# Kernel tuning notes

Hardware: AMD Instinct MI355X
Metric: run time of the kernel (lower is better)

The kernel has to match this reference:

```python
import jax, jax.numpy as jnp
import numpy as np

NUM_HEADS = 16
HEAD_DIM = 80  # head_dim_ori; NPU pads 80->128 with zeros (math-neutral)


def _rotate_half(x):
    x1, x2 = jnp.split(x, 2, axis=-1)
    return jnp.concatenate([-x2, x1], axis=-1)


def setup_inputs() -> dict:
    key = jax.random.key(0)
    ks = jax.random.split(key, 7)
    S, E = 4096, 1280
    inv = jnp.asarray(1.0 / np.sqrt(E), jnp.float32)
    # rotary tables: proper cos/sin from angles for realism
    pos = jnp.arange(S, dtype=jnp.float32)[:, None]
    freqs = 1.0 / (10000.0 ** (jnp.arange(0, HEAD_DIM // 2, dtype=jnp.float32) / (HEAD_DIM // 2)))
    ang = pos * freqs[None, :]                      # [S, 40]
    ang = jnp.concatenate([ang, ang], axis=-1)      # [S, 80] rotate-half layout
    return {
        'hidden_states': jax.random.normal(ks[0], (S, E), jnp.float32),
        'cos': jnp.cos(ang),
        'sin': jnp.sin(ang),
        'w_qkv': jax.random.normal(ks[1], (3 * E, E), jnp.float32) * inv,
        'b_qkv': jax.random.normal(ks[2], (3 * E,), jnp.float32) * 0.02,
        'w_proj': jax.random.normal(ks[3], (E, E), jnp.float32) * inv,
        'b_proj': jax.random.normal(ks[4], (E,), jnp.float32) * 0.02,
    }


def reference(hidden_states, cos, sin, w_qkv, b_qkv, w_proj, b_proj):
    S, E = hidden_states.shape
    H, D = NUM_HEADS, HEAD_DIM
    # fused QKV linear (transposeB=True, hasBias=True) then split into 3
    qkv = hidden_states @ w_qkv.T + b_qkv          # [S, 3E]
    q, k, v = jnp.split(qkv, 3, axis=-1)
    q = q.reshape(S, H, D)
    k = k.reshape(S, H, D)
    v = v.reshape(S, H, D)
    # rotate-half RoPE (rotaryCoeff=2) on q and k
    c = cos[:, None, :]
    s = sin[:, None, :]
    q = q * c + _rotate_half(q) * s
    k = k * c + _rotate_half(k) * s
    # full bidirectional self-attention (PA_ENCODER), qkScale = 1/sqrt(head_dim_ori)
    scale = jnp.asarray(1.0 / np.sqrt(D), q.dtype)
    scores = jnp.einsum('shd,thd->hst', q, k) * scale   # [H, S, S]
    attn = jax.nn.softmax(scores, axis=-1)
    out = jnp.einsum('hst,thd->shd', attn, v).reshape(S, E)
    # output projection + residual add (atten_res_add)
    dense = out @ w_proj.T + b_proj
    return hidden_states + dense
```

## Files before the change

### kernel.cpp

```cpp
#include <hip/hip_runtime.h>
#include <hip/hip_bf16.h>


#define S_LEN 4096
#define E_DIM 1280
#define NH 16
#define HD 80
#define HDP 96

typedef __bf16 bf16x8 __attribute__((ext_vector_type(8)));
typedef float f32x4 __attribute__((ext_vector_type(4)));

__device__ __forceinline__ short f2bf(float x) {
    __hip_bfloat16 h = __float2bfloat16(x);
    return __builtin_bit_cast(short, h);
}
__device__ __forceinline__ bf16x8 ldb(const short* p) {
    return *reinterpret_cast<const bf16x8*>(p);
}
__device__ __forceinline__ unsigned cvt_pk_bf16(float a, float b) {
    unsigned r;
    asm("v_cvt_pk_bf16_f32 %0, %1, %2" : "=v"(r) : "v"(a), "v"(b));
    return r;
}
__device__ __forceinline__ void gload16(const void* g, void* l) {
    __builtin_amdgcn_global_load_lds(
        (const __attribute__((address_space(1))) unsigned int*)g,
        (__attribute__((address_space(3))) unsigned int*)l, 16, 0, 0);
}

__global__ __launch_bounds__(256) void cast3_k(const float* __restrict__ a, short* __restrict__ oa, int na4,
                                               const float* __restrict__ b, short* __restrict__ ob, int nb4,
                                               const float* __restrict__ c, short* __restrict__ oc, int nc4) {
    int j = blockIdx.x * 256 + threadIdx.x;
    const float* src;
    short* dst;
    bool remap = false;
    if (j < na4) {
        src = a; dst = oa;
    } else {
        j -= na4;
        if (j < nb4) {
            src = b; dst = ob; remap = true;
        } else {
            j -= nb4;
            if (j >= nc4) return;
            src = c; dst = oc;
        }
    }
    float4 v = *reinterpret_cast<const float4*>(&src[j * 4]);
    int dj = j;
    if (remap) {
        int row = j / 320, c4 = j - row * 320;
        if (row < 2560) {
            int part = row / 1280;
            int loc = row - part * 1280;
            int hh = loc / 80, d = loc - hh * 80;
            int dp = (d < 40) ? 2 * d : 2 * (d - 40) + 1;
            dj = (part * 1280 + hh * 80 + dp) * 320 + c4;
        }
    }
    ushort4 o;
    o.x = (unsigned short)f2bf(v.x);
    o.y = (unsigned short)f2bf(v.y);
    o.z = (unsigned short)f2bf(v.z);
    o.w = (unsigned short)f2bf(v.w);
    *reinterpret_cast<ushort4*>(&dst[dj * 4]) = o;
}

__global__ __launch_bounds__(512, 2) void gemm1_256_k(
    const short* __restrict__ A, const short* __restrict__ B, const float* __restrict__ bias,
    const float* __restrict__ cosp, const float* __restrict__ sinp,
    short* __restrict__ Qg, short* __restrict__ Kg, short* __restrict__ Vg) {
    const int K = E_DIM;
    __shared__ short As[2][2][8192];
    __shared__ short Bs[2][2][8192];
    int t = threadIdx.x;
    int lane = t & 63, w = t >> 6;
    int wr = w >> 2, wc = w & 3;
    int lr = lane & 15, lg = lane >> 4;
    int bid = blockIdx.x;
    int swz = (bid & 7) * 30 + (bid >> 3);
    int bm = swz / 15, bn = swz % 15;
    int mb = bm * 256, nb = bn * 256;

    int lgs = (t & 3) ^ ((t >> 3) & 3);
    const short* aS = A + (size_t)(mb + (t >> 2)) * K + lgs * 8;
    const short* bS = B + (size_t)(nb + (t >> 2)) * K + lgs * 8;
    const int rowStep = 128 * K;

    int aoff[2][4], boff[4];
#pragma unroll
    for (int mq = 0; mq < 2; mq++)
#pragma unroll
        for (int ii = 0; ii < 4; ii++) {
            int r = wr * 128 + mq * 64 + ii * 16 + lr;
            aoff[mq][ii] = r * 32 + ((lg ^ ((r >> 1) & 3)) * 8);
        }
#pragma unroll
    for (int n = 0; n < 4; n++) {
        int r = wc * 64 + n * 16 + lr;
        boff[n] = r * 32 + ((lg ^ ((r >> 1) & 3)) * 8);
    }

    f32x4 acc[8][4];
#pragma unroll
    for (int i = 0; i < 8; i++)
#pragma unroll
        for (int n = 0; n < 4; n++) acc[i][n] = (f32x4){0.f, 0.f, 0.f, 0.f};

#define STG_A(d, kh, kb2)                                              \
    {                                                                  \
        gload16(aS + (kb2) + (kh)*32, &As[d][kh][w * 512]);            \
        gload16(aS + rowStep + (kb2) + (kh)*32, &As[d][kh][4096 + w * 512]); \
    }
#define STG_B(d, kh, kb2)                                              \
    {                                                                  \
        gload16(bS + (kb2) + (kh)*32, &Bs[d][kh][w * 512]);            \
        gload16(bS + rowStep + (kb2) + (kh)*32, &Bs[d][kh][4096 + w * 512]); \
    }

    STG_A(0, 0, 0);
    STG_B(0, 0, 0);
    STG_A(0, 1, 0);
    STG_B(0, 1, 0);
    asm volatile("s_waitcnt vmcnt(4)" ::: "memory");
    __builtin_amdgcn_s_barrier();
    asm volatile("" ::: "memory");

    for (int kb = 0; kb < K; kb += 64) {
        int d = (kb >> 6) & 1;
        int kb2 = kb + 64;
        bool more = kb2 < K;
        bf16x8 af[4], bfr[4];

#pragma unroll
        for (int n = 0; n < 4; n++) bfr[n] = ldb(&Bs[d][0][boff[n]]);
#pragma unroll
        for (int ii = 0; ii < 4; ii++) af[ii] = ldb(&As[d][0][aoff[0][ii]]);
        if (more) STG_A(d ^ 1, 0, kb2);
        __builtin_amdgcn_s_barrier();
        asm volatile("s_waitcnt lgkmcnt(0)" ::: "memory");
        __builtin_amdgcn_sched_barrier(0);
        __builtin_amdgcn_s_setprio(1);
#pragma unroll
        for (int ii = 0; ii < 4; ii++)
#pragma unroll
            for (int n = 0; n < 4; n++)
                acc[ii][n] = __builtin_amdgcn_mfma_f32_16x16x32_bf16(af[ii], bfr[n], acc[ii][n], 0, 0, 0);
        __builtin_amdgcn_s_setprio(0);
        __builtin_amdgcn_s_barrier();
        asm volatile("" ::: "memory");

#pragma unroll
        for (int ii = 0; ii < 4; ii++) af[ii] = ldb(&As[d][0][aoff[1][ii]]);
        if (more) {
            STG_B(d ^ 1, 0, kb2);
            asm volatile("s_waitcnt vmcnt(4)" ::: "memory");
        } else {
            asm volatile("s_waitcnt vmcnt(0)" ::: "memory");
        }
        __builtin_amdgcn_s_barrier();
        asm volatile("s_waitcnt lgkmcnt(0)" ::: "memory");
        __builtin_amdgcn_sched_barrier(0);
        __builtin_amdgcn_s_setprio(1);
#pragma unroll
        for (int ii = 0; ii < 4; ii++)
#pragma unroll
            for (int n = 0; n < 4; n++)
                acc[4 + ii][n] = __builtin_amdgcn_mfma_f32_16x16x32_bf16(af[ii], bfr[n], acc[4 + ii][n], 0, 0, 0);
        __builtin_amdgcn_s_setprio(0);
        __builtin_amdgcn_s_barrier();
        asm volatile("" ::: "memory");

#pragma unroll
        for (int n = 0; n < 4; n++) bfr[n] = ldb(&Bs[d][1][boff[n]]);
#pragma unroll
        for (int ii = 0; ii < 4; ii++) af[ii] = ldb(&As[d][1][aoff[0][ii]]);
        if (more) STG_A(d ^ 1, 1, kb2);
        __builtin_amdgcn_s_barrier();
        asm volatile("s_waitcnt lgkmcnt(0)" ::: "memory");
        __builtin_amdgcn_sched_barrier(0);
        __builtin_amdgcn_s_setprio(1);
#pragma unroll
        for (int ii = 0; ii < 4; ii++)
#pragma unroll
            for (int n = 0; n < 4; n++)
                acc[ii][n] = __builtin_amdgcn_mfma_f32_16x16x32_bf16(af[ii], bfr[n], acc[ii][n], 0, 0, 0);
        __builtin_amdgcn_s_setprio(0);
        __builtin_amdgcn_s_barrier();
        asm volatile("" ::: "memory");

#pragma unroll
        for (int ii = 0; ii < 4; ii++) af[ii] = ldb(&As[d][1][aoff[1][ii]]);
        if (more) {
            STG_B(d ^ 1, 1, kb2);
            asm volatile("s_waitcnt vmcnt(4)" ::: "memory");
        }
        __builtin_amdgcn_s_barrier();
        asm volatile("s_waitcnt lgkmcnt(0)" ::: "memory");
        __builtin_amdgcn_sched_barrier(0);
        __builtin_amdgcn_s_setprio(1);
#pragma unroll
        for (int ii = 0; ii < 4; ii++)
#pragma unroll
            for (int n = 0; n < 4; n++)
                acc[4 + ii][n] = __builtin_amdgcn_mfma_f32_16x16x32_bf16(af[ii], bfr[n], acc[4 + ii][n], 0, 0, 0);
        __builtin_amdgcn_s_setprio(0);
        __builtin_amdgcn_s_barrier();
        asm volatile("" ::: "memory");
    }
#undef STG_A
#undef STG_B

    int part = nb / E_DIM;
    if (part < 2) {
        short* dst = part ? Kg : Qg;
        const float scl = part ? 1.0f : 0.16129849190f;
#pragma unroll
        for (int j = 0; j < 4; j++) {
            int cn = wc * 64 + j * 16 + lr;
            int pcol = nb - part * E_DIM + cn;
            int hh = pcol / 80;
            int dl = pcol - hh * 80;
            int i2 = dl >> 1;
            int parity = dl & 1;
            float bv = bias[part * E_DIM + hh * 80 + (parity ? i2 + 40 : i2)];
            size_t hbase = (size_t)hh * S_LEN * HDP;
#pragma unroll
            for (int i = 0; i < 8; i++) {
#pragma unroll
                for (int r = 0; r < 4; r++) {
                    int s = mb + wr * 128 + (i >> 2) * 64 + (i & 3) * 16 + lg * 4 + r;
                    float v = acc[i][j][r] + bv;
                    float pv = __shfl_xor(v, 1);
                    float cc = cosp[s * HD + i2];
                    float ss = sinp[s * HD + i2];
                    float ov = fmaf(v, cc, parity ? pv * ss : -pv * ss) * scl;
                    size_t rowb = hbase + (size_t)s * HDP;
                    dst[rowb + dl] = f2bf(ov);
                    if (dl >= 64) dst[rowb + dl + 16] = 0;
                }
            }
        }
    } else {
#pragma unroll
        for (int j = 0; j < 4; j++) {
            int cn = wc * 64 + j * 16 + lr;
            float bv = bias[nb + cn];
            int col = nb - 2 * E_DIM + cn;
#pragma unroll
            for (int i = 0; i < 8; i++) {
#pragma unroll
                for (int r = 0; r < 4; r++) {
                    int s = mb + wr * 128 + (i >> 2) * 64 + (i & 3) * 16 + lg * 4 + r;
                    Vg[(size_t)s * E_DIM + col] = f2bf(acc[i][j][r] + bv);
                }
            }
        }
    }
}

__global__ __launch_bounds__(256) void gemm_bt_k(
    const short* __restrict__ A, const short* __restrict__ B, const float* __restrict__ bias,
    const float* __restrict__ resid, float* __restrict__ Out) {
    const int K = E_DIM;
    __shared__ short As[2][128 * 64];
    __shared__ short Bs[2][128 * 64];
    int t = threadIdx.x;
    int lane = t & 63, w = t >> 6;
    int wr = w >> 1, wc = w & 1;
    int lr = lane & 15, lg = lane >> 4;
    int mb = blockIdx.y * 128, nb = blockIdx.x * 128;

    const short* asrc[4];
    const short* bsrc[4];
#pragma unroll
    for (int c = 0; c < 4; c++) {
        int p = c * 256 + t;
        int m = p >> 3;
        int kg = (p & 7) ^ (m & 7);
        asrc[c] = A + (size_t)(mb + m) * K + kg * 8;
        bsrc[c] = B + (size_t)(nb + m) * K + kg * 8;
    }
    int xa = lr & 7;
    int cx0 = ((0 * 4 + lg) ^ xa) * 8;
    int cx1 = ((1 * 4 + lg) ^ xa) * 8;
    int rowA[4], rowB[4];
#pragma unroll
    for (int i = 0; i < 4; i++) {
        rowA[i] = (wr * 64 + i * 16 + lr) * 64;
        rowB[i] = (wc * 64 + i * 16 + lr) * 64;
    }

    f32x4 acc[4][4];
#pragma unroll
    for (int i = 0; i < 4; i++)
#pragma unroll
        for (int j = 0; j < 4; j++) acc[i][j] = (f32x4){0.f, 0.f, 0.f, 0.f};

#define G_STAGE(buf, kb)                                             \
    {                                                                \
        _Pragma("unroll") for (int c = 0; c < 4; c++) {              \
            int ldso = c * 2048 + w * 512;                           \
            gload16(asrc[c] + (kb), &As[buf][ldso]);                 \
            gload16(bsrc[c] + (kb), &Bs[buf][ldso]);                 \
        }                                                            \
    }

    G_STAGE(0, 0);
    asm volatile("s_waitcnt vmcnt(0)" ::: "memory");
    __syncthreads();

    int buf = 0;
    for (int kb = 0; kb < K; kb += 64) {
        if (kb + 64 < K) G_STAGE(buf ^ 1, kb + 64);
        __builtin_amdgcn_s_setprio(1);
#pragma unroll
        for (int kk = 0; kk < 2; kk++) {
            int cx = kk ? cx1 : cx0;
            bf16x8 af[4], bfr[4];
#pragma unroll
            for (int i = 0; i < 4; i++) {
                af[i] = ldb(&As[buf][rowA[i] + cx]);
                bfr[i] = ldb(&Bs[buf][rowB[i] + cx]);
            }
#pragma unroll
            for (int i = 0; i < 4; i++)
#pragma unroll
                for (int j = 0; j < 4; j++)
                    acc[i][j] = __builtin_amdgcn_mfma_f32_16x16x32_bf16(af[i], bfr[j], acc[i][j], 0, 0, 0);
        }
        __builtin_amdgcn_s_setprio(0);
        __syncthreads();
        buf ^= 1;
    }
#undef G_STAGE

#pragma unroll
    for (int j = 0; j < 4; j++) {
        int n = nb + wc * 64 + j * 16 + lr;
        float bv = bias[n];
#pragma unroll
        for (int i = 0; i < 4; i++) {
#pragma unroll
            for (int r = 0; r < 4; r++) {
                int s = mb + wr * 64 + i * 16 + lg * 4 + r;
                Out[s * E_DIM + n] = acc[i][j][r] + bv + resid[s * E_DIM + n];
            }
        }
    }
}

__global__ __launch_bounds__(256) void transpose_v_k(const short* __restrict__ Vg,
                                                     short* __restrict__ Vt) {
    __shared__ short tile[32][33];
    int h = blockIdx.z, sb = blockIdx.x * 32, db = blockIdx.y * 32;
    int t = threadIdx.x;
    for (int e = t; e < 1024; e += 256) {
        int si = e >> 5, dj = e & 31;
        int d = db + dj;
        tile[si][dj] = (d < HD) ? Vg[(size_t)(sb + si) * E_DIM + h * HD + d] : (short)0;
    }
    __syncthreads();
    for (int e = t; e < 1024; e += 256) {
        int di = e >> 5, sj = e & 31;
        int d = db + di;
        int pj = ((sj >> 2) & 3) * 8 + ((sj >> 4) & 1) * 4 + (sj & 3);
        if (d < HD) Vt[(h * HD + d) * S_LEN + sb + pj] = tile[sj][di];
    }
}

__global__ __launch_bounds__(512, 4) void attn_k(const short* __restrict__ Qg,
                                                 const short* __restrict__ Kg,
                                                 const short* __restrict__ Vt,
                                                 short* __restrict__ Ob) {
    __shared__ __align__(16) short smem[24832];
    short* ksb = smem;
    short* vsb = smem + 13312;

    int t = threadIdx.x;
    int lane = t & 63, w = t >> 6;
    int lr = lane & 15, lg = lane >> 4;
    int pairi = w >> 1, half = w & 1;
    int L = blockIdx.x;
    int h = ((L & 7) << 1) | (L >> 8);
    int qb = ((L >> 3) & 31) << 7;

    const short* kgp = Kg + (size_t)h * S_LEN * HDP;
    const short* vgp = Vt + (size_t)h * HD * S_LEN;

    bf16x8 qf[2][3];
#pragma unroll
    for (int qq = 0; qq < 2; qq++) {
        const short* qp = Qg + ((size_t)h * S_LEN + qb + pairi * 32 + qq * 16 + lr) * HDP;
#pragma unroll
        for (int kk = 0; kk < 3; kk++) qf[qq][kk] = ldb(qp + kk * 32 + lg * 8);
    }
    f32x4 o[2][5];
#pragma unroll
    for (int qq = 0; qq < 2; qq++)
#pragma unroll
        for (int nd = 0; nd < 5; nd++) o[qq][nd] = (f32x4){0.f, 0.f, 0.f, 0.f};
    f32x4 l4[2] = {(f32x4){0.f, 0.f, 0.f, 0.f}, (f32x4){0.f, 0.f, 0.f, 0.f}};

    int gk0 = t, rk0 = gk0 / 13, ok0 = gk0 % 13;
    if (ok0 == 12) ok0 = 0;
    const short* ksrc0 = kgp + rk0 * HDP + ok0 * 8;
    int gk1 = t + 512, rk1 = gk1 / 13, ok1 = gk1 % 13;
    if (ok1 == 12) ok1 = 0;
    const short* ksrc1 = kgp + rk1 * HDP + ok1 * 8;
    int gv0 = t, rv0 = gv0 / 9, ov0 = gv0 % 9;
    if (ov0 == 8) ov0 = 0;
    const short* vsrc0 = vgp + (size_t)rv0 * S_LEN + ov0 * 8;
    bool v1v = (t + 512) < 720;
    int gv1 = t + 512, rv1 = gv1 / 9, ov1 = gv1 % 9;
    if (ov1 == 8) ov1 = 0;
    const short* vsrc1 = vgp + (size_t)rv1 * S_LEN + ov1 * 8;

#define A_STAGE(buf, kb)                                                          \
    {                                                                             \
        gload16(ksrc0 + (size_t)(kb) * HDP, ksb + (buf)*6656 + w * 512);          \
        if (w < 5) gload16(ksrc1 + (size_t)(kb) * HDP, ksb + (buf)*6656 + 4096 + w * 512); \
        gload16(vsrc0 + (kb), vsb + (buf)*5760 + w * 512);                        \
        if (v1v) gload16(vsrc1 + (kb), vsb + (buf)*5760 + 4096 + w * 512);        \
    }

    A_STAGE(0, 0);
    asm volatile("s_waitcnt vmcnt(0)" ::: "memory");
    __syncthreads();

    int buf = 0;
    for (int kb = 0; kb < S_LEN; kb += 64) {
        if (kb + 64 < S_LEN) A_STAGE(buf ^ 1, kb + 64);
        const short* ks = ksb + buf * 6656;
        const short* vs = vsb + buf * 5760;

        f32x4 sc[2][2];
#pragma unroll
        for (int qq = 0; qq < 2; qq++)
#pragma unroll
            for (int n = 0; n < 2; n++) sc[qq][n] = (f32x4){0.f, 0.f, 0.f, 0.f};
        __builtin_amdgcn_s_setprio(1);
#pragma unroll
        for (int n = 0; n < 2; n++) {
#pragma unroll
            for (int kk = 0; kk < 3; kk++) {
                bf16x8 kf = ldb(&ks[(half * 32 + n * 16 + lr) * 104 + kk * 32 + lg * 8]);
                sc[0][n] = __builtin_amdgcn_mfma_f32_16x16x32_bf16(kf, qf[0][kk], sc[0][n], 0, 0, 0);
                sc[1][n] = __builtin_amdgcn_mfma_f32_16x16x32_bf16(kf, qf[1][kk], sc[1][n], 0, 0, 0);
            }
        }
        __builtin_amdgcn_s_setprio(0);

        bf16x8 pa[2];
#pragma unroll
        for (int qq = 0; qq < 2; qq++) {
#pragma unroll
            for (int n = 0; n < 2; n++) {
#pragma unroll
                for (int r = 0; r < 4; r++) sc[qq][n][r] = __builtin_amdgcn_exp2f(sc[qq][n][r]);
                l4[qq] += sc[qq][n];
            }
            uint4 pw;
            pw.x = cvt_pk_bf16(sc[qq][0][0], sc[qq][0][1]);
            pw.y = cvt_pk_bf16(sc[qq][0][2], sc[qq][0][3]);
            pw.z = cvt_pk_bf16(sc[qq][1][0], sc[qq][1][1]);
            pw.w = cvt_pk_bf16(sc[qq][1][2], sc[qq][1][3]);
            pa[qq] = __builtin_bit_cast(bf16x8, pw);
        }

        __builtin_amdgcn_s_setprio(1);
#pragma unroll
        for (int nd = 0; nd < 5; nd++) {
            bf16x8 vf = ldb(&vs[(nd * 16 + lr) * 72 + half * 32 + lg * 8]);
            o[0][nd] = __builtin_amdgcn_mfma_f32_16x16x32_bf16(pa[0], vf, o[0][nd], 0, 0, 0);
            o[1][nd] = __builtin_amdgcn_mfma_f32_16x16x32_bf16(pa[1], vf, o[1][nd], 0, 0, 0);
        }
        __builtin_amdgcn_s_setprio(0);

        __syncthreads();
        buf ^= 1;
    }
#undef A_STAGE

    float lh[2];
#pragma unroll
    for (int qq = 0; qq < 2; qq++) {
        float l = l4[qq][0] + l4[qq][1] + l4[qq][2] + l4[qq][3];
        l += __shfl_xor(l, 16);
        l += __shfl_xor(l, 32);
        lh[qq] = l;
    }
    float* Osc = reinterpret_cast<float*>(smem);
    float* lsc = reinterpret_cast<float*>(smem) + 10240;
    if (half) {
#pragma unroll
        for (int qq = 0; qq < 2; qq++) {
#pragma unroll
            for (int nd = 0; nd < 5; nd++)
#pragma unroll
                for (int r = 0; r < 4; r++)
                    Osc[(pairi * 32 + qq * 16 + lg * 4 + r) * 80 + nd * 16 + lr] = o[qq][nd][r];
            if (lg == 0) lsc[pairi * 32 + qq * 16 + lr] = lh[qq];
        }
    }
    __syncthreads();
    if (!half) {
        float rl[2][4];
#pragma unroll
        for (int qq = 0; qq < 2; qq++) {
            float lt = lh[qq] + lsc[pairi * 32 + qq * 16 + lr];
#pragma unroll
            for (int r = 0; r < 4; r++) {
                float lf = __shfl(lt, lg * 4 + r);
                rl[qq][r] = __builtin_amdgcn_rcpf(lf);
            }
        }
#pragma unroll
        for (int qq = 0; qq < 2; qq++)
#pragma unroll
            for (int nd = 0; nd < 5; nd++)
#pragma unroll
                for (int r = 0; r < 4; r++) {
                    int s = qb + pairi * 32 + qq * 16 + lg * 4 + r;
                    float val = o[qq][nd][r] + Osc[(pairi * 32 + qq * 16 + lg * 4 + r) * 80 + nd * 16 + lr];
                    Ob[s * E_DIM + h * HD + nd * 16 + lr] = f2bf(val * rl[qq][r]);
                }
    }
}

extern "C" void kernel_launch(void* const* d_in, const int* in_sizes, int n_in,
                              void* d_out, int out_size, void* d_ws, size_t ws_size,
                              hipStream_t stream) {
    const float* hidden = (const float*)d_in[0];
    const float* cosp = (const float*)d_in[1];
    const float* sinp = (const float*)d_in[2];
    const float* wqkv = (const float*)d_in[3];
    const float* bqkv = (const float*)d_in[4];
    const float* wproj = (const float*)d_in[5];
    const float* bproj = (const float*)d_in[6];
    float* out = (float*)d_out;

    char* p = (char*)d_ws;
    short* Xb = (short*)p;      p += (size_t)S_LEN * E_DIM * 2;
    short* Wqkvb = (short*)p;   p += (size_t)3 * E_DIM * E_DIM * 2;
    short* Wprojb = (short*)p;  p += (size_t)E_DIM * E_DIM * 2;
    short* Vg = (short*)p;      p += (size_t)S_LEN * E_DIM * 2;
    short* Qg = (short*)p;      p += (size_t)NH * S_LEN * HDP * 2;
    short* Kg = (short*)p;      p += (size_t)NH * S_LEN * HDP * 2;
    short* Vt = (short*)p;      p += (size_t)NH * HD * S_LEN * 2;
    short* Ob = Xb;

    const int na4 = S_LEN * E_DIM / 4;
    const int nb4 = 3 * E_DIM * E_DIM / 4;
    const int nc4 = E_DIM * E_DIM / 4;
    cast3_k<<<(na4 + nb4 + nc4 + 255) / 256, 256, 0, stream>>>(
        hidden, Xb, na4, wqkv, Wqkvb, nb4, wproj, Wprojb, nc4);

    gemm1_256_k<<<dim3(240), 512, 0, stream>>>(Xb, Wqkvb, bqkv, cosp, sinp, Qg, Kg, Vg);

    transpose_v_k<<<dim3(S_LEN / 32, 3, NH), 256, 0, stream>>>(Vg, Vt);

    attn_k<<<dim3(512), 512, 0, stream>>>(Qg, Kg, Vt, Ob);

    gemm_bt_k<<<dim3(E_DIM / 128, S_LEN / 128), 256, 0, stream>>>(
        Ob, Wprojb, bproj, hidden, out);
}
```

Baseline: 209.2 us.

## Stage QKV GEMM epilogue through LDS for vectorized RoPE and stores

The QKV GEMM epilogue now adds bias, converts the accumulators to bf16 and writes them into the reused shared memory with a swizzle. Each thread then reads 8 contiguous columns and applies RoPE with float4 cos/sin loads, writing 16-byte vector stores instead of scattered 2-byte stores and shuffles. Zeroing of the Q/K head-dim padding moves into the cast kernel. This adds a block-wide sync and rounds to bf16 once before RoPE, a small change in precision.

```diff
diff --git a/kernel.cpp b/kernel.cpp
--- a/kernel.cpp
+++ b/kernel.cpp
@@ -15,6 +15,9 @@
     __hip_bfloat16 h = __float2bfloat16(x);
     return __builtin_bit_cast(short, h);
 }
+__device__ __forceinline__ float bf2f(short x) {
+    return __bfloat162float(__builtin_bit_cast(__hip_bfloat16, x));
+}
 __device__ __forceinline__ bf16x8 ldb(const short* p) {
     return *reinterpret_cast<const bf16x8*>(p);
 }
@@ -31,7 +34,8 @@
 
 __global__ __launch_bounds__(256) void cast3_k(const float* __restrict__ a, short* __restrict__ oa, int na4,
                                                const float* __restrict__ b, short* __restrict__ ob, int nb4,
-                                               const float* __restrict__ c, short* __restrict__ oc, int nc4) {
+                                               const float* __restrict__ c, short* __restrict__ oc, int nc4,
+                                               short* __restrict__ Qg, short* __restrict__ Kg, int nd4) {
     int j = blockIdx.x * 256 + threadIdx.x;
     const float* src;
     short* dst;
@@ -44,8 +48,19 @@
             src = b; dst = ob; remap = true;
         } else {
             j -= nb4;
-            if (j >= nc4) return;
-            src = c; dst = oc;
+            if (j < nc4) {
+                src = c; dst = oc;
+            } else {
+                j -= nc4;
+                if (j >= nd4) return;
+                int half = nd4 >> 1;
+                short* base = (j < half) ? Qg : Kg;
+                int rem = (j < half) ? j : j - half;
+                int hs = rem >> 1, gp = rem & 1;
+                int4 z = {0, 0, 0, 0};
+                *reinterpret_cast<int4*>(&base[(size_t)hs * HDP + 80 + gp * 8]) = z;
+                return;
+            }
         }
     }
     float4 v = *reinterpret_cast<const float4*>(&src[j * 4]);
@@ -73,8 +88,9 @@
     const float* __restrict__ cosp, const float* __restrict__ sinp,
     short* __restrict__ Qg, short* __restrict__ Kg, short* __restrict__ Vg) {
     const int K = E_DIM;
-    __shared__ short As[2][2][8192];
-    __shared__ short Bs[2][2][8192];
+    __shared__ __align__(16) short smem[65536];
+#define AS_(d, kh) (smem + (d)*16384 + (kh)*8192)
+#define BS_(d, kh) (smem + 32768 + (d)*16384 + (kh)*8192)
     int t = threadIdx.x;
     int lane = t & 63, w = t >> 6;
     int wr = w >> 2, wc = w & 3;
@@ -111,13 +127,13 @@
 
 #define STG_A(d, kh, kb2)                                              \
     {                                                                  \
-        gload16(aS + (kb2) + (kh)*32, &As[d][kh][w * 512]);            \
-        gload16(aS + rowStep + (kb2) + (kh)*32, &As[d][kh][4096 + w * 512]); \
+        gload16(aS + (kb2) + (kh)*32, AS_(d, kh) + w * 512);           \
+        gload16(aS + rowStep + (kb2) + (kh)*32, AS_(d, kh) + 4096 + w * 512); \
     }
 #define STG_B(d, kh, kb2)                                              \
     {                                                                  \
-        gload16(bS + (kb2) + (kh)*32, &Bs[d][kh][w * 512]);            \
-        gload16(bS + rowStep + (kb2) + (kh)*32, &Bs[d][kh][4096 + w * 512]); \
+        gload16(bS + (kb2) + (kh)*32, BS_(d, kh) + w * 512);           \
+        gload16(bS + rowStep + (kb2) + (kh)*32, BS_(d, kh) + 4096 + w * 512); \
     }
 
     STG_A(0, 0, 0);
@@ -135,9 +151,9 @@
         bf16x8 af[4], bfr[4];
 
 #pragma unroll
-        for (int n = 0; n < 4; n++) bfr[n] = ldb(&Bs[d][0][boff[n]]);
-#pragma unroll
-        for (int ii = 0; ii < 4; ii++) af[ii] = ldb(&As[d][0][aoff[0][ii]]);
+        for (int n = 0; n < 4; n++) bfr[n] = ldb(&BS_(d, 0)[boff[n]]);
+#pragma unroll
+        for (int ii = 0; ii < 4; ii++) af[ii] = ldb(&AS_(d, 0)[aoff[0][ii]]);
         if (more) STG_A(d ^ 1, 0, kb2);
         __builtin_amdgcn_s_barrier();
         asm volatile("s_waitcnt lgkmcnt(0)" ::: "memory");
@@ -153,7 +169,7 @@
         asm volatile("" ::: "memory");
 
 #pragma unroll
-        for (int ii = 0; ii < 4; ii++) af[ii] = ldb(&As[d][0][aoff[1][ii]]);
+        for (int ii = 0; ii < 4; ii++) af[ii] = ldb(&AS_(d, 0)[aoff[1][ii]]);
         if (more) {
             STG_B(d ^ 1, 0, kb2);
             asm volatile("s_waitcnt vmcnt(4)" ::: "memory");
@@ -174,9 +190,9 @@
         asm volatile("" ::: "memory");
 
 #pragma unroll
-        for (int n = 0; n < 4; n++) bfr[n] = ldb(&Bs[d][1][boff[n]]);
-#pragma unroll
-        for (int ii = 0; ii < 4; ii++) af[ii] = ldb(&As[d][1][aoff[0][ii]]);
+        for (int n = 0; n < 4; n++) bfr[n] = ldb(&BS_(d, 1)[boff[n]]);
+#pragma unroll
+        for (int ii = 0; ii < 4; ii++) af[ii] = ldb(&AS_(d, 1)[aoff[0][ii]]);
         if (more) STG_A(d ^ 1, 1, kb2);
         __builtin_amdgcn_s_barrier();
         asm volatile("s_waitcnt lgkmcnt(0)" ::: "memory");
@@ -192,7 +208,7 @@
         asm volatile("" ::: "memory");
 
 #pragma unroll
-        for (int ii = 0; ii < 4; ii++) af[ii] = ldb(&As[d][1][aoff[1][ii]]);
+        for (int ii = 0; ii < 4; ii++) af[ii] = ldb(&AS_(d, 1)[aoff[1][ii]]);
         if (more) {
             STG_B(d ^ 1, 1, kb2);
             asm volatile("s_waitcnt vmcnt(4)" ::: "memory");
@@ -214,51 +230,72 @@
 #undef STG_B
 
     int part = nb / E_DIM;
+    int nloc = nb - part * E_DIM;
+#pragma unroll
+    for (int j = 0; j < 4; j++) {
+        int c = wc * 64 + j * 16 + lr;
+        float bv;
+        if (part < 2) {
+            int pcol = nloc + c;
+            int hh = pcol / 80, dl = pcol - hh * 80;
+            bv = bias[part * E_DIM + hh * 80 + ((dl & 1) ? (dl >> 1) + 40 : (dl >> 1))];
+        } else {
+            bv = bias[nb + c];
+        }
+        int cw = c & 7, cg = c >> 3;
+#pragma unroll
+        for (int i = 0; i < 8; i++) {
+#pragma unroll
+            for (int r = 0; r < 4; r++) {
+                int s = wr * 128 + (i >> 2) * 64 + (i & 3) * 16 + lg * 4 + r;
+                smem[s * 256 + (((cg ^ ((s >> 2) & 3)) << 3) | cw)] = f2bf(acc[i][j][r] + bv);
+            }
+        }
+    }
+    __syncthreads();
     if (part < 2) {
         short* dst = part ? Kg : Qg;
-        const float scl = part ? 1.0f : 0.16129849190f;
-#pragma unroll
-        for (int j = 0; j < 4; j++) {
-            int cn = wc * 64 + j * 16 + lr;
-            int pcol = nb - part * E_DIM + cn;
+        const float qs = part ? 1.0f : 0.16129849190f;
+#pragma unroll
+        for (int k = 0; k < 16; k++) {
+            int g = t + k * 512;
+            int row = g >> 5, gc = g & 31;
+            int pg = gc ^ ((row >> 2) & 3);
+            int4 v = *reinterpret_cast<const int4*>(&smem[row * 256 + pg * 8]);
+            int s = mb + row;
+            int pcol = nloc + gc * 8;
             int hh = pcol / 80;
             int dl = pcol - hh * 80;
             int i2 = dl >> 1;
-            int parity = dl & 1;
-            float bv = bias[part * E_DIM + hh * 80 + (parity ? i2 + 40 : i2)];
-            size_t hbase = (size_t)hh * S_LEN * HDP;
-#pragma unroll
-            for (int i = 0; i < 8; i++) {
-#pragma unroll
-                for (int r = 0; r < 4; r++) {
-                    int s = mb + wr * 128 + (i >> 2) * 64 + (i & 3) * 16 + lg * 4 + r;
-                    float v = acc[i][j][r] + bv;
-                    float pv = __shfl_xor(v, 1);
-                    float cc = cosp[s * HD + i2];
-                    float ss = sinp[s * HD + i2];
-                    float ov = fmaf(v, cc, parity ? pv * ss : -pv * ss) * scl;
-                    size_t rowb = hbase + (size_t)s * HDP;
-                    dst[rowb + dl] = f2bf(ov);
-                    if (dl >= 64) dst[rowb + dl + 16] = 0;
-                }
-            }
+            float4 cs = *reinterpret_cast<const float4*>(&cosp[s * HD + i2]);
+            float4 sn = *reinterpret_cast<const float4*>(&sinp[s * HD + i2]);
+            const short* sp = reinterpret_cast<const short*>(&v);
+            float f[8];
+#pragma unroll
+            for (int i = 0; i < 8; i++) f[i] = bf2f(sp[i]);
+            float c0 = cs.x * qs, s0 = sn.x * qs;
+            float c1 = cs.y * qs, s1 = sn.y * qs;
+            float c2 = cs.z * qs, s2 = sn.z * qs;
+            float c3 = cs.w * qs, s3 = sn.w * qs;
+            uint4 pw;
+            pw.x = cvt_pk_bf16(f[0] * c0 - f[1] * s0, f[1] * c0 + f[0] * s0);
+            pw.y = cvt_pk_bf16(f[2] * c1 - f[3] * s1, f[3] * c1 + f[2] * s1);
+            pw.z = cvt_pk_bf16(f[4] * c2 - f[5] * s2, f[5] * c2 + f[4] * s2);
+            pw.w = cvt_pk_bf16(f[6] * c3 - f[7] * s3, f[7] * c3 + f[6] * s3);
+            *reinterpret_cast<uint4*>(&dst[((size_t)hh * S_LEN + s) * HDP + dl]) = pw;
         }
     } else {
 #pragma unroll
-        for (int j = 0; j < 4; j++) {
-            int cn = wc * 64 + j * 16 + lr;
-            float bv = bias[nb + cn];
-            int col = nb - 2 * E_DIM + cn;
-#pragma unroll
-            for (int i = 0; i < 8; i++) {
-#pragma unroll
-                for (int r = 0; r < 4; r++) {
-                    int s = mb + wr * 128 + (i >> 2) * 64 + (i & 3) * 16 + lg * 4 + r;
-                    Vg[(size_t)s * E_DIM + col] = f2bf(acc[i][j][r] + bv);
-                }
-            }
-        }
-    }
+        for (int k = 0; k < 16; k++) {
+            int g = t + k * 512;
+            int row = g >> 5, gc = g & 31;
+            int pg = gc ^ ((row >> 2) & 3);
+            int4 v = *reinterpret_cast<const int4*>(&smem[row * 256 + pg * 8]);
+            *reinterpret_cast<int4*>(&Vg[(size_t)(mb + row) * E_DIM + nloc + gc * 8]) = v;
+        }
+    }
+#undef AS_
+#undef BS_
 }
 
 __global__ __launch_bounds__(256) void gemm_bt_k(
@@ -555,8 +592,9 @@
     const int na4 = S_LEN * E_DIM / 4;
     const int nb4 = 3 * E_DIM * E_DIM / 4;
     const int nc4 = E_DIM * E_DIM / 4;
-    cast3_k<<<(na4 + nb4 + nc4 + 255) / 256, 256, 0, stream>>>(
-        hidden, Xb, na4, wqkv, Wqkvb, nb4, wproj, Wprojb, nc4);
+    const int nd4 = 2 * NH * S_LEN * 2;
+    cast3_k<<<(na4 + nb4 + nc4 + nd4 + 255) / 256, 256, 0, stream>>>(
+        hidden, Xb, na4, wqkv, Wqkvb, nb4, wproj, Wprojb, nc4, Qg, Kg, nd4);
 
     gemm1_256_k<<<dim3(240), 512, 0, stream>>>(Xb, Wqkvb, bqkv, cosp, sinp, Qg, Kg, Vg);
 
```

New measurement: 187.4 us. -10.4%, faster.
